# Kernel optimization log

Measured on AMD Instinct MI355X. Metric: run time of the kernel, lower is better.

## Reference

```python
import jax, jax.numpy as jnp
import numpy as np
import math

B, LQ, LKV = 8, 1024, 1024
EQ, EKV, H, HD = 1024, 768, 8, 128

def setup_inputs() -> dict:
    key = jax.random.key(0)
    ks = jax.random.split(key, 8)
    def xavier(k, shape, fan_in, fan_out):
        a = math.sqrt(6.0 / (fan_in + fan_out))
        return jax.random.uniform(k, shape, jnp.float32, -a, a)
    return {
        "query": jax.random.normal(ks[0], (B, LQ, EQ), jnp.float32),
        "key": jax.random.normal(ks[1], (B, LKV, EKV), jnp.float32),
        "value": jax.random.normal(ks[2], (B, LKV, EKV), jnp.float32),
        "w_q": xavier(ks[3], (H, EQ, HD), EQ, HD),
        "w_k": xavier(ks[4], (H, EKV, HD), EKV, HD),
        "w_v": xavier(ks[5], (H, EKV, HD), EKV, HD),
        "proj_w": xavier(ks[6], (EQ, H * HD), H * HD, EQ),
        "proj_b": jnp.zeros((EQ,), jnp.float32),
    }

def reference(query, key, value, w_q, w_k, w_v, proj_w, proj_b):
    hd = w_q.shape[-1]
    # per-head projections: [H, B, L, hd]
    q = jnp.einsum('ble,hed->hbld', query, w_q)
    k = jnp.einsum('ble,hed->hbld', key, w_k)
    v = jnp.einsum('ble,hed->hbld', value, w_v)
    # scaled dot-product scores [H, B, Lq, Lkv]
    score = jnp.einsum('hbld,hbmd->hblm', q, k) / jnp.sqrt(jnp.asarray(hd, q.dtype))
    attn = jax.nn.softmax(score, axis=-1)
    out = jnp.einsum('hblm,hbmd->hbld', attn, v)
    # concat heads along feature dim: [B, Lq, H*hd] (head h -> slice h*hd:(h+1)*hd)
    Bsz, Lq = query.shape[0], query.shape[1]
    out = jnp.transpose(out, (1, 2, 0, 3)).reshape(Bsz, Lq, -1)
    out = out @ proj_w.T + proj_b  # dropout is identity at eval
    # torch returns attention_weights as [H*B, Lq, Lkv]
    attn_flat = attn.reshape(-1, attn.shape[-2], attn.shape[-1])
    return out, attn_flat
```

## Files before the change

kernel.cpp:

```cpp
#include <hip/hip_runtime.h>
#include <math.h>


using bf16x8 = __attribute__((ext_vector_type(8))) short;
using f32x4  = __attribute__((ext_vector_type(4))) float;

__device__ __forceinline__ unsigned bf16_rne(float x) {
    unsigned u = __float_as_uint(x);
    return (u + 0x7fffu + ((u >> 16) & 1u)) >> 16;
}

__global__ __launch_bounds__(256) void transpose_k(
    const float* __restrict__ src, float* __restrict__ dst, int R, int C)
{
    __shared__ float tile[32][33];
    const long off = (long)blockIdx.z * R * C;
    src += off; dst += off;
    const int r0 = blockIdx.y * 32, c0 = blockIdx.x * 32;
    const int tx = threadIdx.x & 31, ty = threadIdx.x >> 5;
    #pragma unroll
    for (int i = 0; i < 4; ++i)
        tile[ty + i * 8][tx] = src[(long)(r0 + ty + i * 8) * C + c0 + tx];
    __syncthreads();
    #pragma unroll
    for (int i = 0; i < 4; ++i)
        dst[(long)(c0 + ty + i * 8) * R + r0 + tx] = tile[tx][ty + i * 8];
}

template <bool VT, bool BIAS>
__global__ __launch_bounds__(256, 2) void gemm3(
    const float* __restrict__ A, int lda, long aHS, long aBS,
    const float* __restrict__ Bm, int ldb, long bHS, long bBS,
    float* __restrict__ C, int ldc, long cHS, long cBS,
    int K, float scale, const float* __restrict__ bias)
{
    const int z = blockIdx.z, hh = z >> 3, bb = z & 7;
    A  += (long)hh * aHS + (long)bb * aBS;
    Bm += (long)hh * bHS + (long)bb * bBS;
    C  += (long)hh * cHS + (long)bb * cBS;

    __shared__ short Ahi[128 * 32];
    __shared__ short Alo[128 * 32];
    __shared__ short Bhi[128 * 32];
    __shared__ short Blo[128 * 32];

    const int t    = threadIdx.x;
    const int lane = t & 63, wid = t >> 6;
    const int wr = wid >> 1, wc = wid & 1;
    const int fr = lane & 15, fg = lane >> 4;

    const int m0 = blockIdx.y * 128, n0 = blockIdx.x * 128;

    const int srow = t >> 1;
    const int skh  = (t & 1) << 4;
    const int sb   = srow * 32 + skh;

    f32x4 acc[4][4] = {};

    for (int k0 = 0; k0 < K; k0 += 32) {
        {
            const float* g = A + (long)(m0 + srow) * lda + (k0 + skh);
            const float4 f0 = *(const float4*)(g);
            const float4 f1 = *(const float4*)(g + 4);
            const float4 f2 = *(const float4*)(g + 8);
            const float4 f3 = *(const float4*)(g + 12);
            const float fv[16] = {f0.x, f0.y, f0.z, f0.w, f1.x, f1.y, f1.z, f1.w,
                                  f2.x, f2.y, f2.z, f2.w, f3.x, f3.y, f3.z, f3.w};
            bf16x8 h0, l0, h1, l1;
            #pragma unroll
            for (int i = 0; i < 8; ++i) {
                unsigned ha = bf16_rne(fv[i]);
                h0[i] = (short)ha;
                l0[i] = (short)bf16_rne(fv[i] - __uint_as_float(ha << 16));
                unsigned hb = bf16_rne(fv[8 + i]);
                h1[i] = (short)hb;
                l1[i] = (short)bf16_rne(fv[8 + i] - __uint_as_float(hb << 16));
            }
            *(bf16x8*)&Ahi[sb] = h0;  *(bf16x8*)&Ahi[sb + 8] = h1;
            *(bf16x8*)&Alo[sb] = l0;  *(bf16x8*)&Alo[sb + 8] = l1;
        }
        {
            const float* g = Bm + (long)(n0 + srow) * ldb + (k0 + skh);
            const float4 f0 = *(const float4*)(g);
            const float4 f1 = *(const float4*)(g + 4);
            const float4 f2 = *(const float4*)(g + 8);
            const float4 f3 = *(const float4*)(g + 12);
            const float fv[16] = {f0.x, f0.y, f0.z, f0.w, f1.x, f1.y, f1.z, f1.w,
                                  f2.x, f2.y, f2.z, f2.w, f3.x, f3.y, f3.z, f3.w};
            bf16x8 h0, l0, h1, l1;
            #pragma unroll
            for (int i = 0; i < 8; ++i) {
                unsigned ha = bf16_rne(fv[i]);
                h0[i] = (short)ha;
                l0[i] = (short)bf16_rne(fv[i] - __uint_as_float(ha << 16));
                unsigned hb = bf16_rne(fv[8 + i]);
                h1[i] = (short)hb;
                l1[i] = (short)bf16_rne(fv[8 + i] - __uint_as_float(hb << 16));
            }
            *(bf16x8*)&Bhi[sb] = h0;  *(bf16x8*)&Bhi[sb + 8] = h1;
            *(bf16x8*)&Blo[sb] = l0;  *(bf16x8*)&Blo[sb + 8] = l1;
        }
        __syncthreads();

        bf16x8 ah[4], al[4];
        #pragma unroll
        for (int m = 0; m < 4; ++m) {
            const int r = (wr * 64 + m * 16 + fr) * 32 + fg * 8;
            ah[m] = *(const bf16x8*)&Ahi[r];
            al[m] = *(const bf16x8*)&Alo[r];
        }
        #pragma unroll
        for (int n = 0; n < 4; ++n) {
            const int r = (wc * 64 + n * 16 + fr) * 32 + fg * 8;
            const bf16x8 bh = *(const bf16x8*)&Bhi[r];
            const bf16x8 bl = *(const bf16x8*)&Blo[r];
            #pragma unroll
            for (int m = 0; m < 4; ++m) {
                acc[m][n] = __builtin_amdgcn_mfma_f32_16x16x32_bf16(ah[m], bh, acc[m][n], 0, 0, 0);
                acc[m][n] = __builtin_amdgcn_mfma_f32_16x16x32_bf16(ah[m], bl, acc[m][n], 0, 0, 0);
                acc[m][n] = __builtin_amdgcn_mfma_f32_16x16x32_bf16(al[m], bh, acc[m][n], 0, 0, 0);
            }
        }
        __syncthreads();
    }

    #pragma unroll
    for (int m = 0; m < 4; ++m) {
        const int row0 = m0 + wr * 64 + m * 16 + fg * 4;
        #pragma unroll
        for (int n = 0; n < 4; ++n) {
            const int col = n0 + wc * 64 + n * 16 + fr;
            const f32x4 v = acc[m][n];
            if (VT) {
                float4 w4;
                w4.x = v[0] * scale; w4.y = v[1] * scale;
                w4.z = v[2] * scale; w4.w = v[3] * scale;
                *(float4*)&C[(long)col * ldc + row0] = w4;
            } else {
                const float bv = BIAS ? bias[col] : 0.0f;
                #pragma unroll
                for (int i = 0; i < 4; ++i)
                    C[(long)(row0 + i) * ldc + col] = v[i] * scale + bv;
            }
        }
    }
}

__global__ __launch_bounds__(256) void softmax_rows(float* __restrict__ attn)
{
    const long row = blockIdx.x;
    float* p = attn + row * 1024 + (long)threadIdx.x * 4;
    float4 v = *reinterpret_cast<float4*>(p);

    float m = fmaxf(fmaxf(v.x, v.y), fmaxf(v.z, v.w));
    #pragma unroll
    for (int off = 32; off > 0; off >>= 1)
        m = fmaxf(m, __shfl_down(m, off));

    __shared__ float red[4];
    const int wave = threadIdx.x >> 6, lane = threadIdx.x & 63;
    if (lane == 0) red[wave] = m;
    __syncthreads();
    m = fmaxf(fmaxf(red[0], red[1]), fmaxf(red[2], red[3]));
    __syncthreads();

    v.x = __expf(v.x - m); v.y = __expf(v.y - m);
    v.z = __expf(v.z - m); v.w = __expf(v.w - m);
    float s = v.x + v.y + v.z + v.w;
    #pragma unroll
    for (int off = 32; off > 0; off >>= 1)
        s += __shfl_down(s, off);
    if (lane == 0) red[wave] = s;
    __syncthreads();
    s = red[0] + red[1] + red[2] + red[3];

    const float r = 1.0f / s;
    v.x *= r; v.y *= r; v.z *= r; v.w *= r;
    *reinterpret_cast<float4*>(p) = v;
}

extern "C" void kernel_launch(void* const* d_in, const int* in_sizes, int n_in,
                              void* d_out, int out_size, void* d_ws, size_t ws_size,
                              hipStream_t stream)
{
    const float* query  = (const float*)d_in[0];
    const float* key    = (const float*)d_in[1];
    const float* value  = (const float*)d_in[2];
    const float* w_q    = (const float*)d_in[3];
    const float* w_k    = (const float*)d_in[4];
    const float* w_v    = (const float*)d_in[5];
    const float* proj_w = (const float*)d_in[6];
    const float* proj_b = (const float*)d_in[7];

    float* out  = (float*)d_out;
    float* attn = out + (size_t)8 * 1024 * 1024;

    const size_t SZ = (size_t)8 * 1024 * 1024;
    float* bufQ  = (float*)d_ws;
    float* bufK  = bufQ + SZ;
    float* bufVT = bufK + SZ;
    float* wTq   = bufVT + SZ;
    float* wTk   = wTq + (size_t)8 * 128 * 1024;
    float* wTv   = wTk + (size_t)8 * 128 * 768;
    float* bufO  = bufQ;

    const dim3 blk(256);
    const float isq = 0.08838834764831845f;

    transpose_k<<<dim3(4, 32, 8), blk, 0, stream>>>(w_q, wTq, 1024, 128);
    transpose_k<<<dim3(4, 24, 8), blk, 0, stream>>>(w_k, wTk, 768, 128);
    transpose_k<<<dim3(4, 24, 8), blk, 0, stream>>>(w_v, wTv, 768, 128);

    gemm3<false, false><<<dim3(1, 8, 64), blk, 0, stream>>>(
        query, 1024, 0L, 1048576L,
        wTq,   1024, 131072L, 0L,
        bufQ,  128,  1048576L, 131072L,
        1024, 1.0f, nullptr);

    gemm3<false, false><<<dim3(1, 8, 64), blk, 0, stream>>>(
        key,  768, 0L, (long)1024 * 768,
        wTk,  768, (long)128 * 768, 0L,
        bufK, 128, 1048576L, 131072L,
        768, 1.0f, nullptr);

    gemm3<true, false><<<dim3(1, 8, 64), blk, 0, stream>>>(
        value, 768, 0L, (long)1024 * 768,
        wTv,   768, (long)128 * 768, 0L,
        bufVT, 1024, 1048576L, 131072L,
        768, 1.0f, nullptr);

    gemm3<false, false><<<dim3(8, 8, 64), blk, 0, stream>>>(
        bufQ, 128, 1048576L, 131072L,
        bufK, 128, 1048576L, 131072L,
        attn, 1024, (long)8 * 1048576, 1048576L,
        128, isq, nullptr);

    softmax_rows<<<65536, blk, 0, stream>>>(attn);

    gemm3<false, false><<<dim3(1, 8, 64), blk, 0, stream>>>(
        attn,  1024, (long)8 * 1048576, 1048576L,
        bufVT, 1024, 1048576L, 131072L,
        bufO,  1024, 128L, 1048576L,
        1024, 1.0f, nullptr);

    gemm3<false, true><<<dim3(8, 64, 1), blk, 0, stream>>>(
        bufO,   1024, 0L, 0L,
        proj_w, 1024, 0L, 0L,
        out,    1024, 0L, 0L,
        1024, 1.0f, proj_b);
}
```

Baseline: 883.5 us.

## Pre-split operands into bf16 hi/lo planes and load tiles via global_load_lds

Inputs and weights are split into bf16 hi/lo arrays once in separate passes. GEMM epilogues now write split bf16 outputs directly, so the main GEMMs load pre-split tiles with direct global-to-LDS loads instead of redoing fp32-to-bf16 conversion for every tile. The 1/sqrt(d) scale moves into the Q projection. In exchange there are extra split passes and more scratch memory, part of it placed temporarily in the attention output buffer. The LDS layout for the direct loads has to match what the MFMA reads expect.

```diff
diff --git a/kernel.cpp b/kernel.cpp
--- a/kernel.cpp
+++ b/kernel.cpp
@@ -10,12 +10,40 @@
     return (u + 0x7fffu + ((u >> 16) & 1u)) >> 16;
 }
 
-__global__ __launch_bounds__(256) void transpose_k(
-    const float* __restrict__ src, float* __restrict__ dst, int R, int C)
+#define AS1 __attribute__((address_space(1)))
+#define AS3 __attribute__((address_space(3)))
+
+__device__ __forceinline__ void gl_lds16(const short* g, short* l) {
+    __builtin_amdgcn_global_load_lds((AS1 unsigned*)g, (AS3 unsigned*)l, 16, 0, 0);
+}
+
+__global__ __launch_bounds__(256) void split_f32(
+    const float* __restrict__ src, short* __restrict__ hi,
+    short* __restrict__ lo)
+{
+    const long i = ((long)blockIdx.x * 256 + threadIdx.x) * 8;
+    const float4 a = *(const float4*)(src + i);
+    const float4 b = *(const float4*)(src + i + 4);
+    const float fv[8] = {a.x, a.y, a.z, a.w, b.x, b.y, b.z, b.w};
+    bf16x8 h, l;
+    #pragma unroll
+    for (int j = 0; j < 8; ++j) {
+        unsigned hb = bf16_rne(fv[j]);
+        h[j] = (short)hb;
+        l[j] = (short)bf16_rne(fv[j] - __uint_as_float(hb << 16));
+    }
+    *(bf16x8*)(hi + i) = h;
+    *(bf16x8*)(lo + i) = l;
+}
+
+__global__ __launch_bounds__(256) void transpose_split(
+    const float* __restrict__ src, short* __restrict__ dhi,
+    short* __restrict__ dlo, int R, int C)
 {
     __shared__ float tile[32][33];
-    const long off = (long)blockIdx.z * R * C;
-    src += off; dst += off;
+    src += (long)blockIdx.z * R * C;
+    dhi += (long)blockIdx.z * R * C;
+    dlo += (long)blockIdx.z * R * C;
     const int r0 = blockIdx.y * 32, c0 = blockIdx.x * 32;
     const int tx = threadIdx.x & 31, ty = threadIdx.x >> 5;
     #pragma unroll
@@ -23,26 +51,31 @@
         tile[ty + i * 8][tx] = src[(long)(r0 + ty + i * 8) * C + c0 + tx];
     __syncthreads();
     #pragma unroll
-    for (int i = 0; i < 4; ++i)
-        dst[(long)(c0 + ty + i * 8) * R + r0 + tx] = tile[tx][ty + i * 8];
-}
-
-template <bool VT, bool BIAS>
-__global__ __launch_bounds__(256, 2) void gemm3(
-    const float* __restrict__ A, int lda, long aHS, long aBS,
-    const float* __restrict__ Bm, int ldb, long bHS, long bBS,
-    float* __restrict__ C, int ldc, long cHS, long cBS,
+    for (int i = 0; i < 4; ++i) {
+        const float v = tile[tx][ty + i * 8];
+        const unsigned h = bf16_rne(v);
+        const long o = (long)(c0 + ty + i * 8) * R + r0 + tx;
+        dhi[o] = (short)h;
+        dlo[o] = (short)bf16_rne(v - __uint_as_float(h << 16));
+    }
+}
+
+template <bool AF32, int EP, bool BIAS>
+__global__ __launch_bounds__(256, 2) void gemm_bb(
+    const void* __restrict__ A0, const void* __restrict__ A1, int lda, long aHS, long aBS,
+    const short* __restrict__ B0, const short* __restrict__ B1, int ldb, long bHS, long bBS,
+    void* __restrict__ C0, void* __restrict__ C1, int ldc, long cHS, long cBS,
     int K, float scale, const float* __restrict__ bias)
 {
     const int z = blockIdx.z, hh = z >> 3, bb = z & 7;
-    A  += (long)hh * aHS + (long)bb * aBS;
-    Bm += (long)hh * bHS + (long)bb * bBS;
-    C  += (long)hh * cHS + (long)bb * cBS;
-
-    __shared__ short Ahi[128 * 32];
-    __shared__ short Alo[128 * 32];
-    __shared__ short Bhi[128 * 32];
-    __shared__ short Blo[128 * 32];
+    const long aoff = (long)hh * aHS + (long)bb * aBS;
+    const long boff = (long)hh * bHS + (long)bb * bBS;
+    const long coff = (long)hh * cHS + (long)bb * cBS;
+
+    __shared__ short lAhi[4096];
+    __shared__ short lAlo[4096];
+    __shared__ short lBhi[4096];
+    __shared__ short lBlo[4096];
 
     const int t    = threadIdx.x;
     const int lane = t & 63, wid = t >> 6;
@@ -51,15 +84,22 @@
 
     const int m0 = blockIdx.y * 128, n0 = blockIdx.x * 128;
 
+    const short* Bh = B0 + boff;
+    const short* Bl = B1 + boff;
+    const short* Ah = AF32 ? nullptr : (const short*)A0 + aoff;
+    const short* Al = AF32 ? nullptr : (const short*)A1 + aoff;
+    const float* Af = AF32 ? (const float*)A0 + aoff : nullptr;
+
+    const int glrow = (lane >> 2);
+    const int glk   = (lane & 3) * 8;
     const int srow = t >> 1;
-    const int skh  = (t & 1) << 4;
-    const int sb   = srow * 32 + skh;
+    const int shalf = (t & 1) * 16;
 
     f32x4 acc[4][4] = {};
 
     for (int k0 = 0; k0 < K; k0 += 32) {
-        {
-            const float* g = A + (long)(m0 + srow) * lda + (k0 + skh);
+        if (AF32) {
+            const float* g = Af + (long)(m0 + srow) * lda + k0 + shalf;
             const float4 f0 = *(const float4*)(g);
             const float4 f1 = *(const float4*)(g + 4);
             const float4 f2 = *(const float4*)(g + 8);
@@ -76,49 +116,44 @@
                 h1[i] = (short)hb;
                 l1[i] = (short)bf16_rne(fv[8 + i] - __uint_as_float(hb << 16));
             }
-            *(bf16x8*)&Ahi[sb] = h0;  *(bf16x8*)&Ahi[sb + 8] = h1;
-            *(bf16x8*)&Alo[sb] = l0;  *(bf16x8*)&Alo[sb + 8] = l1;
-        }
-        {
-            const float* g = Bm + (long)(n0 + srow) * ldb + (k0 + skh);
-            const float4 f0 = *(const float4*)(g);
-            const float4 f1 = *(const float4*)(g + 4);
-            const float4 f2 = *(const float4*)(g + 8);
-            const float4 f3 = *(const float4*)(g + 12);
-            const float fv[16] = {f0.x, f0.y, f0.z, f0.w, f1.x, f1.y, f1.z, f1.w,
-                                  f2.x, f2.y, f2.z, f2.w, f3.x, f3.y, f3.z, f3.w};
-            bf16x8 h0, l0, h1, l1;
+            const int sb = srow * 32 + shalf;
+            *(bf16x8*)&lAhi[sb] = h0;  *(bf16x8*)&lAhi[sb + 8] = h1;
+            *(bf16x8*)&lAlo[sb] = l0;  *(bf16x8*)&lAlo[sb + 8] = l1;
+        } else {
             #pragma unroll
-            for (int i = 0; i < 8; ++i) {
-                unsigned ha = bf16_rne(fv[i]);
-                h0[i] = (short)ha;
-                l0[i] = (short)bf16_rne(fv[i] - __uint_as_float(ha << 16));
-                unsigned hb = bf16_rne(fv[8 + i]);
-                h1[i] = (short)hb;
-                l1[i] = (short)bf16_rne(fv[8 + i] - __uint_as_float(hb << 16));
+            for (int j = 0; j < 2; ++j) {
+                const int rowb = wid * 32 + j * 16 + glrow;
+                const long go = (long)(m0 + rowb) * lda + k0 + glk;
+                gl_lds16(Ah + go, &lAhi[(wid * 2 + j) * 512]);
+                gl_lds16(Al + go, &lAlo[(wid * 2 + j) * 512]);
             }
-            *(bf16x8*)&Bhi[sb] = h0;  *(bf16x8*)&Bhi[sb + 8] = h1;
-            *(bf16x8*)&Blo[sb] = l0;  *(bf16x8*)&Blo[sb + 8] = l1;
+        }
+        #pragma unroll
+        for (int j = 0; j < 2; ++j) {
+            const int rowb = wid * 32 + j * 16 + glrow;
+            const long go = (long)(n0 + rowb) * ldb + k0 + glk;
+            gl_lds16(Bh + go, &lBhi[(wid * 2 + j) * 512]);
+            gl_lds16(Bl + go, &lBlo[(wid * 2 + j) * 512]);
         }
         __syncthreads();
 
-        bf16x8 ah[4], al[4];
+        bf16x8 va[4], wa[4];
         #pragma unroll
         for (int m = 0; m < 4; ++m) {
-            const int r = (wr * 64 + m * 16 + fr) * 32 + fg * 8;
-            ah[m] = *(const bf16x8*)&Ahi[r];
-            al[m] = *(const bf16x8*)&Alo[r];
+            const int off = (wr * 64 + m * 16 + fr) * 32 + fg * 8;
+            va[m] = *(const bf16x8*)&lAhi[off];
+            wa[m] = *(const bf16x8*)&lAlo[off];
         }
         #pragma unroll
         for (int n = 0; n < 4; ++n) {
-            const int r = (wc * 64 + n * 16 + fr) * 32 + fg * 8;
-            const bf16x8 bh = *(const bf16x8*)&Bhi[r];
-            const bf16x8 bl = *(const bf16x8*)&Blo[r];
+            const int off = (wc * 64 + n * 16 + fr) * 32 + fg * 8;
+            const bf16x8 vb = *(const bf16x8*)&lBhi[off];
+            const bf16x8 wb = *(const bf16x8*)&lBlo[off];
             #pragma unroll
             for (int m = 0; m < 4; ++m) {
-                acc[m][n] = __builtin_amdgcn_mfma_f32_16x16x32_bf16(ah[m], bh, acc[m][n], 0, 0, 0);
-                acc[m][n] = __builtin_amdgcn_mfma_f32_16x16x32_bf16(ah[m], bl, acc[m][n], 0, 0, 0);
-                acc[m][n] = __builtin_amdgcn_mfma_f32_16x16x32_bf16(al[m], bh, acc[m][n], 0, 0, 0);
+                acc[m][n] = __builtin_amdgcn_mfma_f32_16x16x32_bf16(va[m], vb, acc[m][n], 0, 0, 0);
+                acc[m][n] = __builtin_amdgcn_mfma_f32_16x16x32_bf16(va[m], wb, acc[m][n], 0, 0, 0);
+                acc[m][n] = __builtin_amdgcn_mfma_f32_16x16x32_bf16(wa[m], vb, acc[m][n], 0, 0, 0);
             }
         }
         __syncthreads();
@@ -131,16 +166,37 @@
         for (int n = 0; n < 4; ++n) {
             const int col = n0 + wc * 64 + n * 16 + fr;
             const f32x4 v = acc[m][n];
-            if (VT) {
-                float4 w4;
-                w4.x = v[0] * scale; w4.y = v[1] * scale;
-                w4.z = v[2] * scale; w4.w = v[3] * scale;
-                *(float4*)&C[(long)col * ldc + row0] = w4;
-            } else {
+            if (EP == 0) {
+                float* C = (float*)C0 + coff;
                 const float bv = BIAS ? bias[col] : 0.0f;
                 #pragma unroll
                 for (int i = 0; i < 4; ++i)
                     C[(long)(row0 + i) * ldc + col] = v[i] * scale + bv;
+            } else if (EP == 1) {
+                short* Chp = (short*)C0 + coff;
+                short* Clp = (short*)C1 + coff;
+                #pragma unroll
+                for (int i = 0; i < 4; ++i) {
+                    const float val = v[i] * scale;
+                    const unsigned h = bf16_rne(val);
+                    const long o = (long)(row0 + i) * ldc + col;
+                    Chp[o] = (short)h;
+                    Clp[o] = (short)bf16_rne(val - __uint_as_float(h << 16));
+                }
+            } else {
+                short* Chp = (short*)C0 + coff;
+                short* Clp = (short*)C1 + coff;
+                short4 hv, lv;
+                const float v0 = v[0] * scale, v1 = v[1] * scale,
+                            v2 = v[2] * scale, v3 = v[3] * scale;
+                unsigned h;
+                h = bf16_rne(v0); hv.x = (short)h; lv.x = (short)bf16_rne(v0 - __uint_as_float(h << 16));
+                h = bf16_rne(v1); hv.y = (short)h; lv.y = (short)bf16_rne(v1 - __uint_as_float(h << 16));
+                h = bf16_rne(v2); hv.z = (short)h; lv.z = (short)bf16_rne(v2 - __uint_as_float(h << 16));
+                h = bf16_rne(v3); hv.w = (short)h; lv.w = (short)bf16_rne(v3 - __uint_as_float(h << 16));
+                const long o = (long)col * ldc + row0;
+                *(short4*)&Chp[o] = hv;
+                *(short4*)&Clp[o] = lv;
             }
         }
     }
@@ -195,57 +251,78 @@
     float* out  = (float*)d_out;
     float* attn = out + (size_t)8 * 1024 * 1024;
 
-    const size_t SZ = (size_t)8 * 1024 * 1024;
-    float* bufQ  = (float*)d_ws;
-    float* bufK  = bufQ + SZ;
-    float* bufVT = bufK + SZ;
-    float* wTq   = bufVT + SZ;
-    float* wTk   = wTq + (size_t)8 * 128 * 1024;
-    float* wTv   = wTk + (size_t)8 * 128 * 768;
-    float* bufO  = bufQ;
+    short* ws   = (short*)d_ws;
+    short* Qhi  = ws;
+    short* Qlo  = Qhi + 8388608;
+    short* Khi  = Qlo + 8388608;
+    short* Klo  = Khi + 8388608;
+    short* VThi = Klo + 8388608;
+    short* VTlo = VThi + 8388608;
+    short* pwh  = VTlo + 8388608;
+    short* pwl  = pwh + 1048576;
+    short* Ohi  = Qhi;
+    short* Olo  = Qlo;
+
+    short* sc   = (short*)attn;
+    short* wTqh = sc;
+    short* wTql = wTqh + 1048576;
+    short* wTkh = wTql + 1048576;
+    short* wTkl = wTkh + 786432;
+    short* wTvh = wTkl + 786432;
+    short* wTvl = wTvh + 786432;
+    short* qsh  = wTvl + 786432;
+    short* qsl  = qsh + 8388608;
+    short* ksh  = qsl + 8388608;
+    short* ksl  = ksh + 6291456;
+    short* vsh  = ksl + 6291456;
+    short* vsl  = vsh + 6291456;
 
     const dim3 blk(256);
     const float isq = 0.08838834764831845f;
 
-    transpose_k<<<dim3(4, 32, 8), blk, 0, stream>>>(w_q, wTq, 1024, 128);
-    transpose_k<<<dim3(4, 24, 8), blk, 0, stream>>>(w_k, wTk, 768, 128);
-    transpose_k<<<dim3(4, 24, 8), blk, 0, stream>>>(w_v, wTv, 768, 128);
-
-    gemm3<false, false><<<dim3(1, 8, 64), blk, 0, stream>>>(
-        query, 1024, 0L, 1048576L,
-        wTq,   1024, 131072L, 0L,
-        bufQ,  128,  1048576L, 131072L,
+    split_f32<<<4096, blk, 0, stream>>>(query, qsh, qsl);
+    split_f32<<<3072, blk, 0, stream>>>(key, ksh, ksl);
+    split_f32<<<3072, blk, 0, stream>>>(value, vsh, vsl);
+    split_f32<<<512,  blk, 0, stream>>>(proj_w, pwh, pwl);
+    transpose_split<<<dim3(4, 32, 8), blk, 0, stream>>>(w_q, wTqh, wTql, 1024, 128);
+    transpose_split<<<dim3(4, 24, 8), blk, 0, stream>>>(w_k, wTkh, wTkl, 768, 128);
+    transpose_split<<<dim3(4, 24, 8), blk, 0, stream>>>(w_v, wTvh, wTvl, 768, 128);
+
+    gemm_bb<false, 1, false><<<dim3(1, 8, 64), blk, 0, stream>>>(
+        qsh, qsl, 1024, 0L, 1048576L,
+        wTqh, wTql, 1024, 131072L, 0L,
+        Qhi, Qlo, 128, 1048576L, 131072L,
+        1024, isq, nullptr);
+
+    gemm_bb<false, 1, false><<<dim3(1, 8, 64), blk, 0, stream>>>(
+        ksh, ksl, 768, 0L, 786432L,
+        wTkh, wTkl, 768, 98304L, 0L,
+        Khi, Klo, 128, 1048576L, 131072L,
+        768, 1.0f, nullptr);
+
+    gemm_bb<false, 2, false><<<dim3(1, 8, 64), blk, 0, stream>>>(
+        vsh, vsl, 768, 0L, 786432L,
+        wTvh, wTvl, 768, 98304L, 0L,
+        VThi, VTlo, 1024, 1048576L, 131072L,
+        768, 1.0f, nullptr);
+
+    gemm_bb<false, 0, false><<<dim3(8, 8, 64), blk, 0, stream>>>(
+        Qhi, Qlo, 128, 1048576L, 131072L,
+        Khi, Klo, 128, 1048576L, 131072L,
+        attn, nullptr, 1024, 8388608L, 1048576L,
+        128, 1.0f, nullptr);
+
+    softmax_rows<<<65536, blk, 0, stream>>>(attn);
+
+    gemm_bb<true, 1, false><<<dim3(1, 8, 64), blk, 0, stream>>>(
+        attn, nullptr, 1024, 8388608L, 1048576L,
+        VThi, VTlo, 1024, 1048576L, 131072L,
+        Ohi, Olo, 1024, 128L, 1048576L,
         1024, 1.0f, nullptr);
 
-    gemm3<false, false><<<dim3(1, 8, 64), blk, 0, stream>>>(
-        key,  768, 0L, (long)1024 * 768,
-        wTk,  768, (long)128 * 768, 0L,
-        bufK, 128, 1048576L, 131072L,
-        768, 1.0f, nullptr);
-
-    gemm3<true, false><<<dim3(1, 8, 64), blk, 0, stream>>>(
-        value, 768, 0L, (long)1024 * 768,
-        wTv,   768, (long)128 * 768, 0L,
-        bufVT, 1024, 1048576L, 131072L,
-        768, 1.0f, nullptr);
-
-    gemm3<false, false><<<dim3(8, 8, 64), blk, 0, stream>>>(
-        bufQ, 128, 1048576L, 131072L,
-        bufK, 128, 1048576L, 131072L,
-        attn, 1024, (long)8 * 1048576, 1048576L,
-        128, isq, nullptr);
-
-    softmax_rows<<<65536, blk, 0, stream>>>(attn);
-
-    gemm3<false, false><<<dim3(1, 8, 64), blk, 0, stream>>>(
-        attn,  1024, (long)8 * 1048576, 1048576L,
-        bufVT, 1024, 1048576L, 131072L,
-        bufO,  1024, 128L, 1048576L,
-        1024, 1.0f, nullptr);
-
-    gemm3<false, true><<<dim3(8, 64, 1), blk, 0, stream>>>(
-        bufO,   1024, 0L, 0L,
-        proj_w, 1024, 0L, 0L,
-        out,    1024, 0L, 0L,
+    gemm_bb<false, 0, true><<<dim3(8, 64, 1), blk, 0, stream>>>(
+        Ohi, Olo, 1024, 0L, 0L,
+        pwh, pwl, 1024, 0L, 0L,
+        out, nullptr, 1024, 0L, 0L,
         1024, 1.0f, proj_b);
 }
```

New measurement: 836.0 us. 1.06x faster.
